# Performance work log

Measured on AMD Instinct MI355X. Metric: run time of the kernel, lower is better.

Reference implementation:

```python
import jax, jax.numpy as jnp
import numpy as np

B, S, D_MODEL, D_SPACE = 4, 2048, 1024, 64
N = 512            # size of each neuron pool (all six equal)
TOTAL = 6 * N      # neuron_emb rows
K = 8              # top_k for all four attention branches
EPS = 1e-8


def topk_sparsify(w, k):
    """Top-k sparsification with renormalization via dense one-hot scatter-sum.
    w: [..., N] softmax probs -> sparse renormalized [..., N]."""
    vals, idx = jax.lax.top_k(w, k)                       # [..., k]
    n = w.shape[-1]
    one_hot = jax.nn.one_hot(idx, n, dtype=w.dtype)       # [..., k, N]
    sparse = (one_hot * vals[..., None]).sum(axis=-2)     # [..., N]
    return sparse / (sparse.sum(axis=-1, keepdims=True) + EPS)


def setup_inputs() -> dict:
    key = jax.random.key(0)
    kx, kw, ke = jax.random.split(key, 3)
    x = jax.random.normal(kx, (B, S, D_MODEL), dtype=jnp.float32)
    W_all = jax.random.normal(kw, (D_MODEL, 6 * D_SPACE), dtype=jnp.float32) * 0.02
    b_all = jnp.zeros((6 * D_SPACE,), dtype=jnp.float32)
    neuron_emb = jax.random.normal(ke, (TOTAL, D_SPACE), dtype=jnp.float32) * 0.02
    return {"x": x, "W_all": W_all, "b_all": b_all, "neuron_emb": neuron_emb}


def reference(x, W_all, b_all, neuron_emb):
    # L2-normalized neuron embeddings (cosine-sim logits)
    emb = neuron_emb / (jnp.linalg.norm(neuron_emb, axis=-1, keepdims=True) + EPS)
    # dense projection, then split into 6 heads of d_space (deterministic: no dropout)
    proj = x @ W_all + b_all                              # [B,S,6*d_space]
    h = jnp.split(proj, 6, axis=-1)
    # neuron_emb segments: fqk, fv, rqk, rv (knowledge segments unused here)
    segs = [emb[0:N], emb[0:N], emb[N:2 * N], emb[2 * N:3 * N], emb[2 * N:3 * N], emb[3 * N:4 * N]]
    weights = []
    for hi, ei in zip(h, segs):
        logits = jnp.einsum('bsd,nd->bsn', hi, ei)        # [B,S,N]
        pref = jax.nn.softmax(logits, axis=-1)
        weights.append(topk_sparsify(pref, K))
    # [6, B, S, N]: (fqk_Q, fqk_K, fv, rqk_Q, rqk_K, rv)
    return jnp.stack(weights, axis=0)
```

## Files before the change

kernel.cpp:

```cpp
#include <hip/hip_runtime.h>
#include <math.h>

#define NB 4
#define NS 2048
#define DMODEL 1024
#define DSPACE 64
#define NPOOL 512
#define NHEADS 6
#define NTOK (NB * NS)
#define PROJN (NHEADS * DSPACE)
#define EPSF 1e-8f

typedef float f32x2 __attribute__((ext_vector_type(2)));

#define PK_LO(ACC, A2, B2) \
    asm("v_pk_fma_f32 %0, %1, %2, %0 op_sel:[0,0,0] op_sel_hi:[1,0,1]" \
        : "+v"(ACC) : "v"(A2), "v"(B2))
#define PK_HI(ACC, A2, B2) \
    asm("v_pk_fma_f32 %0, %1, %2, %0 op_sel:[0,1,0] op_sel_hi:[1,1,1]" \
        : "+v"(ACC) : "v"(A2), "v"(B2))

__global__ __launch_bounds__(256) void k_norm_emb(const float* __restrict__ emb,
                                                  float* __restrict__ embT) {
    int row  = blockIdx.x * 4 + (threadIdx.x >> 6);
    int lane = threadIdx.x & 63;
    float v  = emb[row * DSPACE + lane];
    float ss = v * v;
#pragma unroll
    for (int off = 32; off >= 1; off >>= 1) ss += __shfl_xor(ss, off, 64);
    float nrm = sqrtf(ss) + EPSF;
    embT[lane * 2048 + row] = v / nrm;
}

__global__ __launch_bounds__(128, 4) void k_proj(const float* __restrict__ X,
                                                 const float* __restrict__ W,
                                                 const float* __restrict__ bias,
                                                 float* __restrict__ P, int KS) {
    __shared__ float Xt[2][16 * 128];
    __shared__ float Wt[2][16 * 64];
    const int tid = threadIdx.x;
    const int bm  = blockIdx.x * 128;
    const int bn  = blockIdx.y * 64;
    const int z   = blockIdx.z;
    float* Pp = P + (size_t)z * NTOK * PROJN;

    const int r0  = (tid >> 3) << 2;
    const int c0  = (tid & 7) << 2;
    const int lwr = tid >> 3;
    const int lwc = (tid & 7) << 3;

    const float* Xrow = X + (size_t)(bm + tid) * DMODEL;

    f32x2 acc2[4][8];
#pragma unroll
    for (int p = 0; p < 4; ++p)
#pragma unroll
        for (int j = 0; j < 8; ++j) acc2[p][j] = (f32x2){0.f, 0.f};

    const int nsteps = KS >> 4;
    int k0 = z * KS;
    float4 xr0 = *(const float4*)&Xrow[k0 + 0];
    float4 xr1 = *(const float4*)&Xrow[k0 + 4];
    float4 xr2 = *(const float4*)&Xrow[k0 + 8];
    float4 xr3 = *(const float4*)&Xrow[k0 + 12];
    float4 wg0 = *(const float4*)&W[(size_t)(k0 + lwr) * PROJN + bn + lwc];
    float4 wg1 = *(const float4*)&W[(size_t)(k0 + lwr) * PROJN + bn + lwc + 4];

    {
        float* xb = Xt[0]; float* wb = Wt[0];
        xb[ 0*128+tid]=xr0.x; xb[ 1*128+tid]=xr0.y; xb[ 2*128+tid]=xr0.z; xb[ 3*128+tid]=xr0.w;
        xb[ 4*128+tid]=xr1.x; xb[ 5*128+tid]=xr1.y; xb[ 6*128+tid]=xr1.z; xb[ 7*128+tid]=xr1.w;
        xb[ 8*128+tid]=xr2.x; xb[ 9*128+tid]=xr2.y; xb[10*128+tid]=xr2.z; xb[11*128+tid]=xr2.w;
        xb[12*128+tid]=xr3.x; xb[13*128+tid]=xr3.y; xb[14*128+tid]=xr3.z; xb[15*128+tid]=xr3.w;
        *(float4*)&wb[lwr * 64 + lwc]     = wg0;
        *(float4*)&wb[lwr * 64 + lwc + 4] = wg1;
    }

    for (int s = 0; s < nsteps; ++s) {
        if (s + 1 < nsteps) {
            int k1 = k0 + 16;
            xr0 = *(const float4*)&Xrow[k1 + 0];
            xr1 = *(const float4*)&Xrow[k1 + 4];
            xr2 = *(const float4*)&Xrow[k1 + 8];
            xr3 = *(const float4*)&Xrow[k1 + 12];
            wg0 = *(const float4*)&W[(size_t)(k1 + lwr) * PROJN + bn + lwc];
            wg1 = *(const float4*)&W[(size_t)(k1 + lwr) * PROJN + bn + lwc + 4];
        }
        __syncthreads();
        if (s + 1 < nsteps) {
            float* xb = Xt[(s + 1) & 1]; float* wb = Wt[(s + 1) & 1];
            xb[ 0*128+tid]=xr0.x; xb[ 1*128+tid]=xr0.y; xb[ 2*128+tid]=xr0.z; xb[ 3*128+tid]=xr0.w;
            xb[ 4*128+tid]=xr1.x; xb[ 5*128+tid]=xr1.y; xb[ 6*128+tid]=xr1.z; xb[ 7*128+tid]=xr1.w;
            xb[ 8*128+tid]=xr2.x; xb[ 9*128+tid]=xr2.y; xb[10*128+tid]=xr2.z; xb[11*128+tid]=xr2.w;
            xb[12*128+tid]=xr3.x; xb[13*128+tid]=xr3.y; xb[14*128+tid]=xr3.z; xb[15*128+tid]=xr3.w;
            *(float4*)&wb[lwr * 64 + lwc]     = wg0;
            *(float4*)&wb[lwr * 64 + lwc + 4] = wg1;
        }
        const float* xc = Xt[s & 1];
        const float* wc = Wt[s & 1];
#pragma unroll
        for (int kk = 0; kk < 16; ++kk) {
            float4 a0 = *(const float4*)&xc[kk * 128 + r0];
            float4 a1 = *(const float4*)&xc[kk * 128 + r0 + 64];
            float4 b0 = *(const float4*)&wc[kk * 64 + c0];
            float4 b1 = *(const float4*)&wc[kk * 64 + c0 + 32];
            f32x2 ap0 = (f32x2){a0.x, a0.y};
            f32x2 ap1 = (f32x2){a0.z, a0.w};
            f32x2 ap2 = (f32x2){a1.x, a1.y};
            f32x2 ap3 = (f32x2){a1.z, a1.w};
            f32x2 bq0 = (f32x2){b0.x, b0.y};
            f32x2 bq1 = (f32x2){b0.z, b0.w};
            f32x2 bq2 = (f32x2){b1.x, b1.y};
            f32x2 bq3 = (f32x2){b1.z, b1.w};
#pragma unroll
            for (int p = 0; p < 4; ++p) {
                f32x2 ap = (p == 0) ? ap0 : (p == 1) ? ap1 : (p == 2) ? ap2 : ap3;
                PK_LO(acc2[p][0], ap, bq0); PK_HI(acc2[p][1], ap, bq0);
                PK_LO(acc2[p][2], ap, bq1); PK_HI(acc2[p][3], ap, bq1);
                PK_LO(acc2[p][4], ap, bq2); PK_HI(acc2[p][5], ap, bq2);
                PK_LO(acc2[p][6], ap, bq3); PK_HI(acc2[p][7], ap, bq3);
            }
        }
        k0 += 16;
    }

#pragma unroll
    for (int i = 0; i < 8; ++i) {
        int row = bm + r0 + ((i < 4) ? i : 60 + i);
        float o0[4], o1[4];
#pragma unroll
        for (int j = 0; j < 4; ++j) {
            f32x2 v0 = acc2[i >> 1][j];
            f32x2 v1 = acc2[i >> 1][j + 4];
            o0[j] = (i & 1) ? v0.y : v0.x;
            o1[j] = (i & 1) ? v1.y : v1.x;
        }
        if (z == 0) {
#pragma unroll
            for (int j = 0; j < 4; ++j) {
                o0[j] += bias[bn + c0 + j];
                o1[j] += bias[bn + c0 + 32 + j];
            }
        }
        *(float4*)&Pp[(size_t)row * PROJN + bn + c0]      = *(float4*)&o0[0];
        *(float4*)&Pp[(size_t)row * PROJN + bn + c0 + 32] = *(float4*)&o1[0];
    }
}

__global__ __launch_bounds__(256) void k_sum(float* __restrict__ P, int SK) {
    size_t i = ((size_t)blockIdx.x * 256 + threadIdx.x) * 4;
    float4 v = *(const float4*)&P[i];
    for (int ks = 1; ks < SK; ++ks) {
        float4 u = *(const float4*)&P[(size_t)ks * NTOK * PROJN + i];
        v.x += u.x; v.y += u.y; v.z += u.z; v.w += u.w;
    }
    *(float4*)&P[i] = v;
}

#define CE(arr, a, b) { float _hi = fmaxf(arr[a], arr[b]); arr[b] = fminf(arr[a], arr[b]); arr[a] = _hi; }

#define SORT8(s) \
    CE(s,0,1) CE(s,2,3) CE(s,4,5) CE(s,6,7) \
    CE(s,0,2) CE(s,1,3) CE(s,4,6) CE(s,5,7) \
    CE(s,1,2) CE(s,5,6) \
    CE(s,0,4) CE(s,1,5) CE(s,2,6) CE(s,3,7) \
    CE(s,2,4) CE(s,3,5) \
    CE(s,1,2) CE(s,3,4) CE(s,5,6)

#define SWZ(v, IMM) __int_as_float(__builtin_amdgcn_ds_swizzle(__float_as_int(v), IMM))

#define BFLY_LEVEL(XCHG) { \
    float q[4][8]; \
    _Pragma("unroll") \
    for (int tt = 0; tt < 4; ++tt) { \
        _Pragma("unroll") \
        for (int i = 0; i < 8; ++i) { float _x = s[tt][i]; q[tt][i] = XCHG(_x); } \
    } \
    _Pragma("unroll") \
    for (int tt = 0; tt < 4; ++tt) { \
        float c[8]; \
        c[0] = fmaxf(s[tt][0], q[tt][7]); c[1] = fmaxf(s[tt][1], q[tt][6]); \
        c[2] = fmaxf(s[tt][2], q[tt][5]); c[3] = fmaxf(s[tt][3], q[tt][4]); \
        c[4] = fmaxf(s[tt][4], q[tt][3]); c[5] = fmaxf(s[tt][5], q[tt][2]); \
        c[6] = fmaxf(s[tt][6], q[tt][1]); c[7] = fmaxf(s[tt][7], q[tt][0]); \
        CE(c,0,4) CE(c,1,5) CE(c,2,6) CE(c,3,7) \
        CE(c,0,2) CE(c,1,3) CE(c,4,6) CE(c,5,7) \
        CE(c,0,1) CE(c,2,3) CE(c,4,5) CE(c,6,7) \
        _Pragma("unroll") \
        for (int i = 0; i < 8; ++i) s[tt][i] = c[i]; \
    } }

#define X1(v)  SWZ(v, 0x041F)
#define X2(v)  SWZ(v, 0x081F)
#define X4(v)  SWZ(v, 0x101F)
#define X8(v)  SWZ(v, 0x201F)
#define X16(v) SWZ(v, 0x401F)
#define X32(v) __shfl_xor(v, 32, 64)

__global__ __launch_bounds__(256, 2) void k_router(const float* __restrict__ hfinal,
                                                   const float* __restrict__ embT,
                                                   float* __restrict__ out) {
    const int head = blockIdx.y;
    const int tid  = threadIdx.x;
    const int wid  = tid >> 6;
    const int lane = tid & 63;
    const int so = (head == 2) ? 512 : (head == 3 || head == 4) ? 1024
                 : (head == 5) ? 1536 : 0;

    const int tbase = __builtin_amdgcn_readfirstlane(blockIdx.x * 32 + (wid << 3));
    const float* hrow  = hfinal + (size_t)tbase * PROJN + head * DSPACE;
    const float* ebase = embT + so + (lane << 3);

    float acc[8][8];
#pragma unroll
    for (int t = 0; t < 8; ++t)
#pragma unroll
        for (int j = 0; j < 8; ++j) acc[t][j] = 0.f;

    for (int dc = 0; dc < DSPACE; dc += 2) {
        float e[2][8];
#pragma unroll
        for (int dd = 0; dd < 2; ++dd) {
            const float* er = ebase + (size_t)(dc + dd) * 2048;
            *(float4*)&e[dd][0] = *(const float4*)&er[0];
            *(float4*)&e[dd][4] = *(const float4*)&er[4];
        }
#pragma unroll
        for (int dd = 0; dd < 2; ++dd) {
#pragma unroll
            for (int t = 0; t < 8; ++t) {
                float hv = hrow[t * PROJN + dc + dd];
#pragma unroll
                for (int j = 0; j < 8; ++j) acc[t][j] = fmaf(hv, e[dd][j], acc[t][j]);
            }
        }
    }

    const size_t obase = ((size_t)head * NTOK + tbase) * NPOOL;

#pragma unroll
    for (int g = 0; g < 2; ++g) {
        float l[4][8], s[4][8];
#pragma unroll
        for (int tt = 0; tt < 4; ++tt)
#pragma unroll
            for (int j = 0; j < 8; ++j) {
                l[tt][j] = acc[4 * g + tt][j];
                s[tt][j] = l[tt][j];
            }

        SORT8(s[0]) SORT8(s[1]) SORT8(s[2]) SORT8(s[3])

        BFLY_LEVEL(X1)
        BFLY_LEVEL(X2)
        BFLY_LEVEL(X4)
        BFLY_LEVEL(X8)
        BFLY_LEVEL(X16)
        BFLY_LEVEL(X32)

        unsigned gtm[4], eqm[4]; int own[4], inc[4];
#pragma unroll
        for (int tt = 0; tt < 4; ++tt) {
            const float T = s[tt][7];
            unsigned g_ = 0, e_ = 0; int cg = 0, ce = 0;
#pragma unroll
            for (int j = 0; j < 8; ++j) {
                if (l[tt][j] > T)       { g_ |= 1u << j; ++cg; }
                else if (l[tt][j] == T) { e_ |= 1u << j; ++ce; }
            }
            gtm[tt] = g_; eqm[tt] = e_;
            own[tt] = (ce << 8) | cg;
            inc[tt] = own[tt];
        }
#pragma unroll
        for (int off = 1; off < 64; off <<= 1) {
            int v0 = __shfl_up(inc[0], off, 64);
            int v1 = __shfl_up(inc[1], off, 64);
            int v2 = __shfl_up(inc[2], off, 64);
            int v3 = __shfl_up(inc[3], off, 64);
            if (lane >= off) { inc[0] += v0; inc[1] += v1; inc[2] += v2; inc[3] += v3; }
        }

#pragma unroll
        for (int tt = 0; tt < 4; ++tt) {
            const float T = s[tt][7];
            const float m = s[tt][0];
            int tot  = __shfl(inc[tt], 63, 64);
            int need = 8 - (tot & 0xff);
            int eqpre = (inc[tt] - own[tt]) >> 8;
            unsigned sel = gtm[tt];
#pragma unroll
            for (int j = 0; j < 8; ++j) {
                if ((eqm[tt] >> j) & 1u) { if (eqpre < need) sel |= 1u << j; ++eqpre; }
            }

            float s8 = 0.f;
#pragma unroll
            for (int i = 0; i < 8; ++i) s8 += __expf(s[tt][i] - m);
            float invd = 1.0f / s8;

            float o[8];
#pragma unroll
            for (int j = 0; j < 8; ++j)
                o[j] = ((sel >> j) & 1u) ? __expf(l[tt][j] - m) * invd : 0.0f;
            float4* dst = (float4*)&out[obase + (size_t)(4 * g + tt) * NPOOL + (lane << 3)];
            dst[0] = *(float4*)&o[0];
            dst[1] = *(float4*)&o[4];
        }
    }
}

extern "C" void kernel_launch(void* const* d_in, const int* in_sizes, int n_in,
                              void* d_out, int out_size, void* d_ws, size_t ws_size,
                              hipStream_t stream) {
    const float* x   = (const float*)d_in[0];
    const float* W   = (const float*)d_in[1];
    const float* b   = (const float*)d_in[2];
    const float* emb = (const float*)d_in[3];
    float* out  = (float*)d_out;
    float* embT = (float*)d_ws;
    float* proj = embT + 64 * 2048;

    size_t base = (size_t)64 * 2048 * 4;
    size_t slab = (size_t)NTOK * PROJN * 4;
    int SK = (ws_size >= base + 4 * slab) ? 4
           : (ws_size >= base + 2 * slab) ? 2 : 1;
    int KS = DMODEL / SK;

    k_norm_emb<<<dim3(512), dim3(256), 0, stream>>>(emb, embT);
    dim3 g2(NTOK / 128, PROJN / 64, SK);
    k_proj<<<g2, dim3(128), 0, stream>>>(x, W, b, proj, KS);
    if (SK > 1)
        k_sum<<<dim3(NTOK * PROJN / 4 / 256), dim3(256), 0, stream>>>(proj, SK);
    dim3 g3(NTOK / 32, NHEADS);
    k_router<<<g3, dim3(256), 0, stream>>>(proj, embT, out);
}
```

Baseline: 181.7 us.

## Rewrite projection GEMM with wave-uniform scalar W loads and drop split-K reduction

Replaces the register-tiled packed-FMA projection GEMM with a kernel where each wave owns 16 output columns. W rows are read through wave-uniform addresses, which lets them be served by scalar loads, and only X is staged in LDS. The split-K path and its separate reduction kernel are removed, so one launch and the partial-sum traffic go away. In exchange each thread does 16 FMAs per LDS read with one row and no 2D register blocking, which lowers arithmetic intensity and may make the GEMM slower if scalar load latency or LDS bandwidth becomes the limit.

Measured after the change: 196.4 us. 1.08x slower.

```diff
diff --git a/kernel.cpp b/kernel.cpp
--- a/kernel.cpp
+++ b/kernel.cpp
@@ -11,15 +11,6 @@
 #define PROJN (NHEADS * DSPACE)
 #define EPSF 1e-8f
 
-typedef float f32x2 __attribute__((ext_vector_type(2)));
-
-#define PK_LO(ACC, A2, B2) \
-    asm("v_pk_fma_f32 %0, %1, %2, %0 op_sel:[0,0,0] op_sel_hi:[1,0,1]" \
-        : "+v"(ACC) : "v"(A2), "v"(B2))
-#define PK_HI(ACC, A2, B2) \
-    asm("v_pk_fma_f32 %0, %1, %2, %0 op_sel:[0,1,0] op_sel_hi:[1,1,1]" \
-        : "+v"(ACC) : "v"(A2), "v"(B2))
-
 __global__ __launch_bounds__(256) void k_norm_emb(const float* __restrict__ emb,
                                                   float* __restrict__ embT) {
     int row  = blockIdx.x * 4 + (threadIdx.x >> 6);
@@ -32,129 +23,78 @@
     embT[lane * 2048 + row] = v / nrm;
 }
 
-__global__ __launch_bounds__(128, 4) void k_proj(const float* __restrict__ X,
-                                                 const float* __restrict__ W,
-                                                 const float* __restrict__ bias,
-                                                 float* __restrict__ P, int KS) {
-    __shared__ float Xt[2][16 * 128];
-    __shared__ float Wt[2][16 * 64];
-    const int tid = threadIdx.x;
-    const int bm  = blockIdx.x * 128;
-    const int bn  = blockIdx.y * 64;
-    const int z   = blockIdx.z;
-    float* Pp = P + (size_t)z * NTOK * PROJN;
-
-    const int r0  = (tid >> 3) << 2;
-    const int c0  = (tid & 7) << 2;
-    const int lwr = tid >> 3;
-    const int lwc = (tid & 7) << 3;
-
-    const float* Xrow = X + (size_t)(bm + tid) * DMODEL;
-
-    f32x2 acc2[4][8];
-#pragma unroll
-    for (int p = 0; p < 4; ++p)
-#pragma unroll
-        for (int j = 0; j < 8; ++j) acc2[p][j] = (f32x2){0.f, 0.f};
-
-    const int nsteps = KS >> 4;
-    int k0 = z * KS;
-    float4 xr0 = *(const float4*)&Xrow[k0 + 0];
-    float4 xr1 = *(const float4*)&Xrow[k0 + 4];
-    float4 xr2 = *(const float4*)&Xrow[k0 + 8];
-    float4 xr3 = *(const float4*)&Xrow[k0 + 12];
-    float4 wg0 = *(const float4*)&W[(size_t)(k0 + lwr) * PROJN + bn + lwc];
-    float4 wg1 = *(const float4*)&W[(size_t)(k0 + lwr) * PROJN + bn + lwc + 4];
+__global__ __launch_bounds__(256) void k_proj(const float* __restrict__ X,
+                                              const float* __restrict__ W,
+                                              const float* __restrict__ bias,
+                                              float* __restrict__ P) {
+    __shared__ float Xt[2][32 * 64];
+    const int tid  = threadIdx.x;
+    const int bm   = blockIdx.x * 64;
+    const int bn   = blockIdx.y * 64;
+    const int lane = tid & 63;
+    const int cbase = __builtin_amdgcn_readfirstlane(bn + (tid >> 6) * 16);
+    const int srow = tid & 63;
+    const int skk  = (tid >> 6) << 3;
+    const float* Xrow = X + (size_t)(bm + srow) * DMODEL + skk;
+
+    float acc[16];
+#pragma unroll
+    for (int j = 0; j < 16; ++j) acc[j] = 0.f;
+
+    const int nsteps = DMODEL / 32;
+    float4 xa = *(const float4*)&Xrow[0];
+    float4 xb = *(const float4*)&Xrow[4];
 
     {
-        float* xb = Xt[0]; float* wb = Wt[0];
-        xb[ 0*128+tid]=xr0.x; xb[ 1*128+tid]=xr0.y; xb[ 2*128+tid]=xr0.z; xb[ 3*128+tid]=xr0.w;
-        xb[ 4*128+tid]=xr1.x; xb[ 5*128+tid]=xr1.y; xb[ 6*128+tid]=xr1.z; xb[ 7*128+tid]=xr1.w;
-        xb[ 8*128+tid]=xr2.x; xb[ 9*128+tid]=xr2.y; xb[10*128+tid]=xr2.z; xb[11*128+tid]=xr2.w;
-        xb[12*128+tid]=xr3.x; xb[13*128+tid]=xr3.y; xb[14*128+tid]=xr3.z; xb[15*128+tid]=xr3.w;
-        *(float4*)&wb[lwr * 64 + lwc]     = wg0;
-        *(float4*)&wb[lwr * 64 + lwc + 4] = wg1;
+        float* d = Xt[0];
+        d[(skk + 0) * 64 + srow] = xa.x; d[(skk + 1) * 64 + srow] = xa.y;
+        d[(skk + 2) * 64 + srow] = xa.z; d[(skk + 3) * 64 + srow] = xa.w;
+        d[(skk + 4) * 64 + srow] = xb.x; d[(skk + 5) * 64 + srow] = xb.y;
+        d[(skk + 6) * 64 + srow] = xb.z; d[(skk + 7) * 64 + srow] = xb.w;
     }
 
     for (int s = 0; s < nsteps; ++s) {
         if (s + 1 < nsteps) {
-            int k1 = k0 + 16;
-            xr0 = *(const float4*)&Xrow[k1 + 0];
-            xr1 = *(const float4*)&Xrow[k1 + 4];
-            xr2 = *(const float4*)&Xrow[k1 + 8];
-            xr3 = *(const float4*)&Xrow[k1 + 12];
-            wg0 = *(const float4*)&W[(size_t)(k1 + lwr) * PROJN + bn + lwc];
-            wg1 = *(const float4*)&W[(size_t)(k1 + lwr) * PROJN + bn + lwc + 4];
+            xa = *(const float4*)&Xrow[(s + 1) * 32 + 0];
+            xb = *(const float4*)&Xrow[(s + 1) * 32 + 4];
         }
         __syncthreads();
         if (s + 1 < nsteps) {
-            float* xb = Xt[(s + 1) & 1]; float* wb = Wt[(s + 1) & 1];
-            xb[ 0*128+tid]=xr0.x; xb[ 1*128+tid]=xr0.y; xb[ 2*128+tid]=xr0.z; xb[ 3*128+tid]=xr0.w;
-            xb[ 4*128+tid]=xr1.x; xb[ 5*128+tid]=xr1.y; xb[ 6*128+tid]=xr1.z; xb[ 7*128+tid]=xr1.w;
-            xb[ 8*128+tid]=xr2.x; xb[ 9*128+tid]=xr2.y; xb[10*128+tid]=xr2.z; xb[11*128+tid]=xr2.w;
-            xb[12*128+tid]=xr3.x; xb[13*128+tid]=xr3.y; xb[14*128+tid]=xr3.z; xb[15*128+tid]=xr3.w;
-            *(float4*)&wb[lwr * 64 + lwc]     = wg0;
-            *(float4*)&wb[lwr * 64 + lwc + 4] = wg1;
+            float* d = Xt[(s + 1) & 1];
+            d[(skk + 0) * 64 + srow] = xa.x; d[(skk + 1) * 64 + srow] = xa.y;
+            d[(skk + 2) * 64 + srow] = xa.z; d[(skk + 3) * 64 + srow] = xa.w;
+            d[(skk + 4) * 64 + srow] = xb.x; d[(skk + 5) * 64 + srow] = xb.y;
+            d[(skk + 6) * 64 + srow] = xb.z; d[(skk + 7) * 64 + srow] = xb.w;
         }
         const float* xc = Xt[s & 1];
-        const float* wc = Wt[s & 1];
-#pragma unroll
-        for (int kk = 0; kk < 16; ++kk) {
-            float4 a0 = *(const float4*)&xc[kk * 128 + r0];
-            float4 a1 = *(const float4*)&xc[kk * 128 + r0 + 64];
-            float4 b0 = *(const float4*)&wc[kk * 64 + c0];
-            float4 b1 = *(const float4*)&wc[kk * 64 + c0 + 32];
-            f32x2 ap0 = (f32x2){a0.x, a0.y};
-            f32x2 ap1 = (f32x2){a0.z, a0.w};
-            f32x2 ap2 = (f32x2){a1.x, a1.y};
-            f32x2 ap3 = (f32x2){a1.z, a1.w};
-            f32x2 bq0 = (f32x2){b0.x, b0.y};
-            f32x2 bq1 = (f32x2){b0.z, b0.w};
-            f32x2 bq2 = (f32x2){b1.x, b1.y};
-            f32x2 bq3 = (f32x2){b1.z, b1.w};
-#pragma unroll
-            for (int p = 0; p < 4; ++p) {
-                f32x2 ap = (p == 0) ? ap0 : (p == 1) ? ap1 : (p == 2) ? ap2 : ap3;
-                PK_LO(acc2[p][0], ap, bq0); PK_HI(acc2[p][1], ap, bq0);
-                PK_LO(acc2[p][2], ap, bq1); PK_HI(acc2[p][3], ap, bq1);
-                PK_LO(acc2[p][4], ap, bq2); PK_HI(acc2[p][5], ap, bq2);
-                PK_LO(acc2[p][6], ap, bq3); PK_HI(acc2[p][7], ap, bq3);
-            }
-        }
-        k0 += 16;
-    }
-
-#pragma unroll
-    for (int i = 0; i < 8; ++i) {
-        int row = bm + r0 + ((i < 4) ? i : 60 + i);
-        float o0[4], o1[4];
-#pragma unroll
-        for (int j = 0; j < 4; ++j) {
-            f32x2 v0 = acc2[i >> 1][j];
-            f32x2 v1 = acc2[i >> 1][j + 4];
-            o0[j] = (i & 1) ? v0.y : v0.x;
-            o1[j] = (i & 1) ? v1.y : v1.x;
-        }
-        if (z == 0) {
-#pragma unroll
-            for (int j = 0; j < 4; ++j) {
-                o0[j] += bias[bn + c0 + j];
-                o1[j] += bias[bn + c0 + 32 + j];
-            }
-        }
-        *(float4*)&Pp[(size_t)row * PROJN + bn + c0]      = *(float4*)&o0[0];
-        *(float4*)&Pp[(size_t)row * PROJN + bn + c0 + 32] = *(float4*)&o1[0];
-    }
-}
-
-__global__ __launch_bounds__(256) void k_sum(float* __restrict__ P, int SK) {
-    size_t i = ((size_t)blockIdx.x * 256 + threadIdx.x) * 4;
-    float4 v = *(const float4*)&P[i];
-    for (int ks = 1; ks < SK; ++ks) {
-        float4 u = *(const float4*)&P[(size_t)ks * NTOK * PROJN + i];
-        v.x += u.x; v.y += u.y; v.z += u.z; v.w += u.w;
-    }
-    *(float4*)&P[i] = v;
+        const float* wk = W + (size_t)(s * 32) * PROJN + cbase;
+#pragma unroll
+        for (int kk = 0; kk < 32; ++kk) {
+            float a = xc[kk * 64 + lane];
+            const float* wr = wk + (size_t)kk * PROJN;
+            float4 w0 = *(const float4*)&wr[0];
+            float4 w1 = *(const float4*)&wr[4];
+            float4 w2 = *(const float4*)&wr[8];
+            float4 w3 = *(const float4*)&wr[12];
+            acc[ 0] = fmaf(a, w0.x, acc[ 0]); acc[ 1] = fmaf(a, w0.y, acc[ 1]);
+            acc[ 2] = fmaf(a, w0.z, acc[ 2]); acc[ 3] = fmaf(a, w0.w, acc[ 3]);
+            acc[ 4] = fmaf(a, w1.x, acc[ 4]); acc[ 5] = fmaf(a, w1.y, acc[ 5]);
+            acc[ 6] = fmaf(a, w1.z, acc[ 6]); acc[ 7] = fmaf(a, w1.w, acc[ 7]);
+            acc[ 8] = fmaf(a, w2.x, acc[ 8]); acc[ 9] = fmaf(a, w2.y, acc[ 9]);
+            acc[10] = fmaf(a, w2.z, acc[10]); acc[11] = fmaf(a, w2.w, acc[11]);
+            acc[12] = fmaf(a, w3.x, acc[12]); acc[13] = fmaf(a, w3.y, acc[13]);
+            acc[14] = fmaf(a, w3.z, acc[14]); acc[15] = fmaf(a, w3.w, acc[15]);
+        }
+    }
+
+    float o[16];
+#pragma unroll
+    for (int j = 0; j < 16; ++j) o[j] = acc[j] + bias[cbase + j];
+    float* dst = &P[(size_t)(bm + lane) * PROJN + cbase];
+    *(float4*)&dst[0]  = *(float4*)&o[0];
+    *(float4*)&dst[4]  = *(float4*)&o[4];
+    *(float4*)&dst[8]  = *(float4*)&o[8];
+    *(float4*)&dst[12] = *(float4*)&o[12];
 }
 
 #define CE(arr, a, b) { float _hi = fmaxf(arr[a], arr[b]); arr[b] = fminf(arr[a], arr[b]); arr[a] = _hi; }
@@ -321,17 +261,9 @@
     float* embT = (float*)d_ws;
     float* proj = embT + 64 * 2048;
 
-    size_t base = (size_t)64 * 2048 * 4;
-    size_t slab = (size_t)NTOK * PROJN * 4;
-    int SK = (ws_size >= base + 4 * slab) ? 4
-           : (ws_size >= base + 2 * slab) ? 2 : 1;
-    int KS = DMODEL / SK;
-
     k_norm_emb<<<dim3(512), dim3(256), 0, stream>>>(emb, embT);
-    dim3 g2(NTOK / 128, PROJN / 64, SK);
-    k_proj<<<g2, dim3(128), 0, stream>>>(x, W, b, proj, KS);
-    if (SK > 1)
-        k_sum<<<dim3(NTOK * PROJN / 4 / 256), dim3(256), 0, stream>>>(proj, SK);
+    dim3 g2(NTOK / 64, PROJN / 64);
+    k_proj<<<g2, dim3(256), 0, stream>>>(x, W, b, proj);
     dim3 g3(NTOK / 32, NHEADS);
     k_router<<<g3, dim3(256), 0, stream>>>(proj, embT, out);
 }
```
